# Kernel optimization log

Hardware: AMD Instinct MI355X
Metric: run time of the kernel (lower is better)

## Reference

```python
import jax, jax.numpy as jnp
import numpy as np

N_THRESHOLDS = 10  # module default; thresholds = linspace(0,1,T+2)[1:-1]


def setup_inputs() -> dict:
    key = jax.random.key(0)
    k1, k2, k3 = jax.random.split(key, 3)
    shape = (96, 512, 512)
    prediction = jax.random.normal(k1, shape, dtype=jnp.float32)
    mask = jax.random.uniform(k2, shape) > 0.5
    target = jax.random.uniform(k3, shape) > 0.5
    return {"prediction": prediction, "mask": mask, "target": target}


def reference(prediction, mask, target):
    # thresholds exactly as in the torch module
    thresholds = jnp.linspace(0.0, 1.0, N_THRESHOLDS + 2)[1:-1]  # [T]

    p = jax.nn.sigmoid(prediction).ravel()   # [N] probabilities
    m = mask.ravel()                          # [N] valid-pixel mask
    t = target.ravel() & m                    # [N] positive labels within mask

    # [T, N] predicted-positive per threshold (single fused pass, no host syncs)
    pos = p[None, :] > thresholds[:, None]

    tp = jnp.sum(pos & t[None, :], axis=1)    # [T]
    pos_cnt = jnp.sum(pos & m[None, :], axis=1)  # [T] positives within mask

    n_mask = jnp.sum(m)   # total valid pixels (tp+fp+tn+fn)
    n_tgt = jnp.sum(t)    # total label positives (tp+fn)

    fp = pos_cnt - tp
    fn = n_tgt - tp
    tn = n_mask - pos_cnt - fn

    # classes layout matches torch: rows = [tp, fp, tn, fn], cols = thresholds
    return jnp.stack([tp, fp, tn, fn], axis=0)
```

## Files before the change

kernel.cpp:

```cpp
#include <hip/hip_runtime.h>
#include <math.h>

#define NT 10
#define NC 22
#define BLOCK 256
#define MAXB 2048
#define WS_PART_OFF 64

struct Logits { float L[NT]; };

__global__ void pr_probe(const unsigned char* __restrict__ m,
                         const unsigned char* __restrict__ t,
                         unsigned* __restrict__ flag_out)
{
    const int idx = threadIdx.x;
    unsigned char a = m[idx * 4 + 1];
    unsigned char b = t[idx * 4 + 1];
    unsigned long long bal = __ballot(a | b);
    if (idx == 0) flag_out[0] = bal ? 1u : 0u;
}

__global__ __launch_bounds__(BLOCK) void pr_count(
    const float* __restrict__ pred,
    const void* __restrict__ maskv,
    const void* __restrict__ targv,
    const unsigned* __restrict__ flag_p,
    unsigned* __restrict__ partials,
    int n, Logits lg)
{
    unsigned tp[NT], cnt[NT];
#pragma unroll
    for (int k = 0; k < NT; ++k) { tp[k] = 0u; cnt[k] = 0u; }
    unsigned nm = 0u, ntg = 0u;

    const unsigned flag = flag_p[0];
    const int stride = gridDim.x * blockDim.x;
    const int tid0 = blockIdx.x * blockDim.x + threadIdx.x;
    const int n4 = n >> 2;

    const float4* p4 = (const float4*)pred;

    if (flag) {
        const unsigned* m4 = (const unsigned*)maskv;
        const unsigned* t4 = (const unsigned*)targv;
#pragma unroll 2
        for (int i = tid0; i < n4; i += stride) {
            float4 p = p4[i];
            unsigned mw = m4[i];
            unsigned tw = t4[i];
            float pv[4] = { p.x, p.y, p.z, p.w };
#pragma unroll
            for (int j = 0; j < 4; ++j) {
                unsigned mb = (mw >> (8 * j)) & 0xffu;
                unsigned tb = (tw >> (8 * j)) & 0xffu;
                unsigned mm = mb ? 1u : 0u;
                unsigned tt = (tb && mb) ? 1u : 0u;
                nm += mm; ntg += tt;
#pragma unroll
                for (int k = 0; k < NT; ++k) {
                    bool pos = pv[j] > lg.L[k];
                    cnt[k] += pos ? mm : 0u;
                    tp[k]  += pos ? tt : 0u;
                }
            }
        }
    } else {
        const int4* m4 = (const int4*)maskv;
        const int4* t4 = (const int4*)targv;
#pragma unroll 2
        for (int i = tid0; i < n4; i += stride) {
            float4 p = p4[i];
            int4 m = m4[i];
            int4 t = t4[i];
            float pv[4] = { p.x, p.y, p.z, p.w };
            int   mv[4] = { m.x, m.y, m.z, m.w };
            int   tv[4] = { t.x, t.y, t.z, t.w };
#pragma unroll
            for (int j = 0; j < 4; ++j) {
                unsigned mm = mv[j] ? 1u : 0u;
                unsigned tt = (tv[j] && mv[j]) ? 1u : 0u;
                nm += mm; ntg += tt;
#pragma unroll
                for (int k = 0; k < NT; ++k) {
                    bool pos = pv[j] > lg.L[k];
                    cnt[k] += pos ? mm : 0u;
                    tp[k]  += pos ? tt : 0u;
                }
            }
        }
    }

    if (tid0 == 0) {
        for (int i = n4 * 4; i < n; ++i) {
            unsigned mm, tt;
            if (flag) {
                unsigned mb = ((const unsigned char*)maskv)[i];
                unsigned tb = ((const unsigned char*)targv)[i];
                mm = mb ? 1u : 0u; tt = (tb && mb) ? 1u : 0u;
            } else {
                int mvv = ((const int*)maskv)[i];
                int tvv = ((const int*)targv)[i];
                mm = mvv ? 1u : 0u; tt = (tvv && mvv) ? 1u : 0u;
            }
            nm += mm; ntg += tt;
            for (int k = 0; k < NT; ++k) {
                bool pos = pred[i] > lg.L[k];
                cnt[k] += pos ? mm : 0u;
                tp[k]  += pos ? tt : 0u;
            }
        }
    }

#pragma unroll
    for (int off = 32; off; off >>= 1) {
        nm  += __shfl_down(nm, off);
        ntg += __shfl_down(ntg, off);
#pragma unroll
        for (int k = 0; k < NT; ++k) {
            tp[k]  += __shfl_down(tp[k], off);
            cnt[k] += __shfl_down(cnt[k], off);
        }
    }

    __shared__ unsigned red[BLOCK / 64][NC];
    const int lane = threadIdx.x & 63;
    const int wid = threadIdx.x >> 6;
    if (lane == 0) {
#pragma unroll
        for (int k = 0; k < NT; ++k) {
            red[wid][k] = tp[k];
            red[wid][NT + k] = cnt[k];
        }
        red[wid][20] = nm;
        red[wid][21] = ntg;
    }
    __syncthreads();
    if (threadIdx.x < NC) {
        unsigned s = 0u;
#pragma unroll
        for (int w = 0; w < BLOCK / 64; ++w) s += red[w][threadIdx.x];
        partials[threadIdx.x * gridDim.x + blockIdx.x] = s;
    }
}

__global__ __launch_bounds__(BLOCK) void pr_final(
    const unsigned* __restrict__ partials, int nb, int* __restrict__ out)
{
    __shared__ unsigned wred[NC][BLOCK / 64];
    __shared__ unsigned tot[NC];
    const int tid = threadIdx.x;
    const int lane = tid & 63;
    const int wid = tid >> 6;

    for (int c = 0; c < NC; ++c) {
        unsigned s = 0u;
        for (int i = tid; i < nb; i += BLOCK) s += partials[c * nb + i];
#pragma unroll
        for (int off = 32; off; off >>= 1) s += __shfl_down(s, off);
        if (lane == 0) wred[c][wid] = s;
    }
    __syncthreads();
    if (tid < NC) {
        unsigned s = 0u;
#pragma unroll
        for (int w = 0; w < BLOCK / 64; ++w) s += wred[tid][w];
        tot[tid] = s;
    }
    __syncthreads();
    if (tid < 4 * NT) {
        const int row = tid / NT, k = tid % NT;
        const unsigned tpv = tot[k], cntv = tot[NT + k];
        const unsigned nmv = tot[20], ntgv = tot[21];
        const unsigned fpv = cntv - tpv;
        const unsigned fnv = ntgv - tpv;
        const unsigned tnv = nmv - cntv - fnv;
        unsigned v = (row == 0) ? tpv : (row == 1) ? fpv : (row == 2) ? tnv : fnv;
        out[tid] = (int)v;
    }
}

extern "C" void kernel_launch(void* const* d_in, const int* in_sizes, int n_in,
                              void* d_out, int out_size, void* d_ws, size_t ws_size,
                              hipStream_t stream) {
    const float* pred = (const float*)d_in[0];
    const void* mask = d_in[1];
    const void* targ = d_in[2];
    const int n = in_sizes[0];

    unsigned* flag = (unsigned*)d_ws;
    unsigned* partials = (unsigned*)((char*)d_ws + WS_PART_OFF);

    int nb = MAXB;
    const size_t need_per_block = (size_t)NC * sizeof(unsigned);
    if (ws_size < WS_PART_OFF + (size_t)nb * need_per_block)
        nb = (int)((ws_size - WS_PART_OFF) / need_per_block);
    if (nb < 1) nb = 1;

    Logits lg;
    const float step = 1.0f / 11.0f;
    for (int k = 0; k < NT; ++k) {
        float th = (float)(k + 1) * step;
        double lo = log((double)th / (1.0 - (double)th));
        float L = (float)lo;
        if ((double)L > lo) L = nextafterf(L, -INFINITY);
        lg.L[k] = L;
    }

    pr_probe<<<1, 64, 0, stream>>>((const unsigned char*)mask,
                                   (const unsigned char*)targ, flag);
    pr_count<<<nb, BLOCK, 0, stream>>>(pred, mask, targ, flag, partials, n, lg);
    pr_final<<<1, BLOCK, 0, stream>>>(partials, nb, (int*)d_out);
}
```

Before: 313.9 us.

## Pack tp and mask counts into shared 16-bit halves and widen loads

Result: no change. 312.2 us (-0.5%).

```diff
diff --git a/kernel.cpp b/kernel.cpp
--- a/kernel.cpp
+++ b/kernel.cpp
@@ -4,10 +4,18 @@
 #define NT 10
 #define NC 22
 #define BLOCK 256
-#define MAXB 2048
+#define NBLK 2048
 #define WS_PART_OFF 64
 
 struct Logits { float L[NT]; };
+
+
+static __device__ __forceinline__ unsigned norm01(unsigned x) {
+    unsigned t = x | (x >> 1);
+    t |= t >> 2;
+    t |= t >> 4;
+    return t & 0x01010101u;
+}
 
 __global__ void pr_probe(const unsigned char* __restrict__ m,
                          const unsigned char* __restrict__ t,
@@ -21,105 +29,111 @@
 }
 
 __global__ __launch_bounds__(BLOCK) void pr_count(
-    const float* __restrict__ pred,
+    const float4* __restrict__ pred4,
     const void* __restrict__ maskv,
     const void* __restrict__ targv,
     const unsigned* __restrict__ flag_p,
     unsigned* __restrict__ partials,
     int n, Logits lg)
 {
-    unsigned tp[NT], cnt[NT];
-#pragma unroll
-    for (int k = 0; k < NT; ++k) { tp[k] = 0u; cnt[k] = 0u; }
-    unsigned nm = 0u, ntg = 0u;
+    unsigned combo[NT];
+#pragma unroll
+    for (int k = 0; k < NT; ++k) combo[k] = 0u;
+    unsigned nmtg = 0u;
 
     const unsigned flag = flag_p[0];
     const int stride = gridDim.x * blockDim.x;
     const int tid0 = blockIdx.x * blockDim.x + threadIdx.x;
-    const int n4 = n >> 2;
-
-    const float4* p4 = (const float4*)pred;
-
-    if (flag) {
-        const unsigned* m4 = (const unsigned*)maskv;
-        const unsigned* t4 = (const unsigned*)targv;
-#pragma unroll 2
-        for (int i = tid0; i < n4; i += stride) {
-            float4 p = p4[i];
-            unsigned mw = m4[i];
-            unsigned tw = t4[i];
-            float pv[4] = { p.x, p.y, p.z, p.w };
-#pragma unroll
-            for (int j = 0; j < 4; ++j) {
-                unsigned mb = (mw >> (8 * j)) & 0xffu;
-                unsigned tb = (tw >> (8 * j)) & 0xffu;
-                unsigned mm = mb ? 1u : 0u;
-                unsigned tt = (tb && mb) ? 1u : 0u;
-                nm += mm; ntg += tt;
-#pragma unroll
-                for (int k = 0; k < NT; ++k) {
-                    bool pos = pv[j] > lg.L[k];
-                    cnt[k] += pos ? mm : 0u;
-                    tp[k]  += pos ? tt : 0u;
+
+    if (!flag) {
+        const uint4* m4 = (const uint4*)maskv;
+        const uint4* t4 = (const uint4*)targv;
+        const int n8 = n >> 3;
+        for (int g = tid0; g < n8; g += stride) {
+            float4 p0 = pred4[2 * g + 0];
+            float4 p1 = pred4[2 * g + 1];
+            uint4 mw0 = m4[2 * g + 0];
+            uint4 mw1 = m4[2 * g + 1];
+            uint4 tw0 = t4[2 * g + 0];
+            uint4 tw1 = t4[2 * g + 1];
+            float    pj[8] = { p0.x, p0.y, p0.z, p0.w, p1.x, p1.y, p1.z, p1.w };
+            unsigned mv[8] = { mw0.x, mw0.y, mw0.z, mw0.w, mw1.x, mw1.y, mw1.z, mw1.w };
+            unsigned tv[8] = { tw0.x, tw0.y, tw0.z, tw0.w, tw1.x, tw1.y, tw1.z, tw1.w };
+#pragma unroll
+            for (int j = 0; j < 8; ++j) {
+                unsigned mm = mv[j] ? 1u : 0u;
+                unsigned tt = (mv[j] && tv[j]) ? 1u : 0u;
+                unsigned pair = mm | (tt << 16);
+                nmtg += pair;
+#pragma unroll
+                for (int k = 0; k < NT; ++k)
+                    combo[k] += (pj[j] > lg.L[k]) ? pair : 0u;
+            }
+        }
+        if (tid0 == 0) {
+            const float* pred = (const float*)pred4;
+            const int* m = (const int*)maskv;
+            const int* t = (const int*)targv;
+            for (int i = n8 * 8; i < n; ++i) {
+                unsigned mm = m[i] ? 1u : 0u;
+                unsigned tt = (m[i] && t[i]) ? 1u : 0u;
+                unsigned pair = mm | (tt << 16);
+                nmtg += pair;
+                for (int k = 0; k < NT; ++k)
+                    combo[k] += (pred[i] > lg.L[k]) ? pair : 0u;
+            }
+        }
+    } else {
+        const uint4* m16 = (const uint4*)maskv;
+        const uint4* t16 = (const uint4*)targv;
+        const int n16 = n >> 4;
+        for (int g = tid0; g < n16; g += stride) {
+            float4 p0 = pred4[4 * g + 0];
+            float4 p1 = pred4[4 * g + 1];
+            float4 p2 = pred4[4 * g + 2];
+            float4 p3 = pred4[4 * g + 3];
+            uint4 mwv = m16[g];
+            uint4 twv = t16[g];
+            float4 P[4] = { p0, p1, p2, p3 };
+            unsigned MW[4] = { norm01(mwv.x), norm01(mwv.y), norm01(mwv.z), norm01(mwv.w) };
+            unsigned TW[4] = { norm01(twv.x), norm01(twv.y), norm01(twv.z), norm01(twv.w) };
+#pragma unroll
+            for (int q = 0; q < 4; ++q) {
+                float pj[4] = { P[q].x, P[q].y, P[q].z, P[q].w };
+                const unsigned mword = MW[q], tword = TW[q];
+#pragma unroll
+                for (int j = 0; j < 4; ++j) {
+                    unsigned mb = (mword >> (8 * j)) & 1u;
+                    unsigned tb = (tword >> (8 * j)) & 1u;
+                    unsigned pair = mb | ((mb & tb) << 16);
+                    nmtg += pair;
+#pragma unroll
+                    for (int k = 0; k < NT; ++k)
+                        combo[k] += (pj[j] > lg.L[k]) ? pair : 0u;
                 }
             }
         }
-    } else {
-        const int4* m4 = (const int4*)maskv;
-        const int4* t4 = (const int4*)targv;
-#pragma unroll 2
-        for (int i = tid0; i < n4; i += stride) {
-            float4 p = p4[i];
-            int4 m = m4[i];
-            int4 t = t4[i];
-            float pv[4] = { p.x, p.y, p.z, p.w };
-            int   mv[4] = { m.x, m.y, m.z, m.w };
-            int   tv[4] = { t.x, t.y, t.z, t.w };
-#pragma unroll
-            for (int j = 0; j < 4; ++j) {
-                unsigned mm = mv[j] ? 1u : 0u;
-                unsigned tt = (tv[j] && mv[j]) ? 1u : 0u;
-                nm += mm; ntg += tt;
-#pragma unroll
-                for (int k = 0; k < NT; ++k) {
-                    bool pos = pv[j] > lg.L[k];
-                    cnt[k] += pos ? mm : 0u;
-                    tp[k]  += pos ? tt : 0u;
-                }
-            }
-        }
-    }
-
-    if (tid0 == 0) {
-        for (int i = n4 * 4; i < n; ++i) {
-            unsigned mm, tt;
-            if (flag) {
-                unsigned mb = ((const unsigned char*)maskv)[i];
-                unsigned tb = ((const unsigned char*)targv)[i];
-                mm = mb ? 1u : 0u; tt = (tb && mb) ? 1u : 0u;
-            } else {
-                int mvv = ((const int*)maskv)[i];
-                int tvv = ((const int*)targv)[i];
-                mm = mvv ? 1u : 0u; tt = (tvv && mvv) ? 1u : 0u;
-            }
-            nm += mm; ntg += tt;
-            for (int k = 0; k < NT; ++k) {
-                bool pos = pred[i] > lg.L[k];
-                cnt[k] += pos ? mm : 0u;
-                tp[k]  += pos ? tt : 0u;
+        if (tid0 == 0) {
+            const float* pred = (const float*)pred4;
+            const unsigned char* m = (const unsigned char*)maskv;
+            const unsigned char* t = (const unsigned char*)targv;
+            for (int i = n16 * 16; i < n; ++i) {
+                unsigned mm = m[i] ? 1u : 0u;
+                unsigned tt = (m[i] && t[i]) ? 1u : 0u;
+                unsigned pair = mm | (tt << 16);
+                nmtg += pair;
+                for (int k = 0; k < NT; ++k)
+                    combo[k] += (pred[i] > lg.L[k]) ? pair : 0u;
             }
         }
     }
 
 #pragma unroll
     for (int off = 32; off; off >>= 1) {
-        nm  += __shfl_down(nm, off);
-        ntg += __shfl_down(ntg, off);
-#pragma unroll
-        for (int k = 0; k < NT; ++k) {
-            tp[k]  += __shfl_down(tp[k], off);
-            cnt[k] += __shfl_down(cnt[k], off);
-        }
+        nmtg += __shfl_down(nmtg, off);
+#pragma unroll
+        for (int k = 0; k < NT; ++k)
+            combo[k] += __shfl_down(combo[k], off);
     }
 
     __shared__ unsigned red[BLOCK / 64][NC];
@@ -128,11 +142,11 @@
     if (lane == 0) {
 #pragma unroll
         for (int k = 0; k < NT; ++k) {
-            red[wid][k] = tp[k];
-            red[wid][NT + k] = cnt[k];
-        }
-        red[wid][20] = nm;
-        red[wid][21] = ntg;
+            red[wid][k]      = combo[k] >> 16;
+            red[wid][NT + k] = combo[k] & 0xffffu;
+        }
+        red[wid][20] = nmtg & 0xffffu;
+        red[wid][21] = nmtg >> 16;
     }
     __syncthreads();
     if (threadIdx.x < NC) {
@@ -190,7 +204,7 @@
     unsigned* flag = (unsigned*)d_ws;
     unsigned* partials = (unsigned*)((char*)d_ws + WS_PART_OFF);
 
-    int nb = MAXB;
+    int nb = NBLK;
     const size_t need_per_block = (size_t)NC * sizeof(unsigned);
     if (ws_size < WS_PART_OFF + (size_t)nb * need_per_block)
         nb = (int)((ws_size - WS_PART_OFF) / need_per_block);
@@ -208,6 +222,7 @@
 
     pr_probe<<<1, 64, 0, stream>>>((const unsigned char*)mask,
                                    (const unsigned char*)targ, flag);
-    pr_count<<<nb, BLOCK, 0, stream>>>(pred, mask, targ, flag, partials, n, lg);
+    pr_count<<<nb, BLOCK, 0, stream>>>((const float4*)pred, mask, targ,
+                                       flag, partials, n, lg);
     pr_final<<<1, BLOCK, 0, stream>>>(partials, nb, (int*)d_out);
 }
```
